# Performance work log

Measured on AMD Instinct MI355X. Metric: run time of the kernel, lower is better.

## Reference

```python
import jax, jax.numpy as jnp
import numpy as np

D_MODEL = 768
N_HEADS = 12
D_HEAD = 64
WINDOW = 16
LOOK_BACK = 1
IGNORE = -1.0e6


def look_around(x, backward=LOOK_BACK, forward=0, pad_value=0):
    # x: (b, n_windows, w, ...) -> (b, n_windows, w*(backward+forward+1), ...)
    n = x.shape[1]
    pad = [(0, 0)] * x.ndim
    pad[1] = (backward, forward)
    px = jnp.pad(x, pad, constant_values=pad_value)
    return jnp.concatenate([px[:, i:i + n] for i in range(backward + forward + 1)], axis=2)


def setup_inputs() -> dict:
    key = jax.random.key(0)
    k1, k2, k3 = jax.random.split(key, 3)
    B, T = 2, 2048
    x = jax.random.normal(k1, (B, T, D_MODEL), dtype=jnp.float32)
    W_abcde = jax.random.normal(k2, (D_MODEL, 5 * N_HEADS * D_HEAD), dtype=jnp.float32) * (1.0 / np.sqrt(D_MODEL))
    b_abcde = jnp.zeros((5 * N_HEADS * D_HEAD,), dtype=jnp.float32)
    W_O = jax.random.normal(k3, (N_HEADS * D_HEAD, D_MODEL), dtype=jnp.float32) * (1.0 / np.sqrt(N_HEADS * D_HEAD))
    b_O = jnp.zeros((D_MODEL,), dtype=jnp.float32)
    return {"x": x, "W_abcde": W_abcde, "b_abcde": b_abcde, "W_O": W_O, "b_O": b_O}


def reference(x, W_abcde, b_abcde, W_O, b_O):
    B, T, _ = x.shape
    w = WINDOW
    nw = T // w
    Ww = w * (LOOK_BACK + 1)  # look-around window length

    abcde = x @ W_abcde + b_abcde                                    # (B,T,5*H*D)
    abcde = abcde.reshape(B, T, 5, N_HEADS, D_HEAD).transpose(2, 0, 3, 1, 4)  # (5,B,H,T,D)
    a, b, c, d, e = [t.reshape(B * N_HEADS, nw, w, D_HEAD) for t in abcde]
    a_l, b_l, d_l, e_l = (look_around(t) for t in (a, b, d, e))       # (BH,nw,Ww,D)

    # causal mask, same construction as get_causal_mask (pad_value=0)
    seq = jnp.arange(T).reshape(1, nw, w)
    bb = look_around(seq)                                            # (1,nw,Ww)
    # mask[n,m,l] = (seq_n < bb_l) | (bb_l <= bb_m)
    mask = (seq[..., :, None, None] < bb[..., None, None, :]) | (bb[..., None, None, :] <= bb[..., None, :, None])

    # third-order attention scores: (BH, nw, w, Ww, Ww)
    scores = jnp.einsum('bnwd,bnmd,bnld->bnwml', c, a_l, b_l)
    scores = jnp.where(mask, IGNORE, scores)
    scores = jnp.where(scores == 0, IGNORE, scores)
    probs = jax.nn.softmax((scores / D_HEAD).reshape(B * N_HEADS, nw, w, Ww * Ww), axis=-1)
    probs = probs.reshape(scores.shape)

    z = jnp.einsum('bnwml,bnmd->bnwd', probs, d_l) + jnp.einsum('bnwml,bnld->bnwd', probs, e_l)
    z = z.reshape(B, N_HEADS, nw, w, D_HEAD).transpose(0, 2, 3, 1, 4).reshape(B, T, N_HEADS * D_HEAD)
    return z @ W_O + b_O
```

## Files before the change

kernel.cpp:

```cpp
#include <hip/hip_runtime.h>

#define T_SEQ   2048
#define NHEADS  12
#define DHEAD   64
#define WIN     16
#define WW      32
#define NWIN    128
#define DMODEL  768
#define NABCDE  3840
#define IGNORE_V (-1.0e6f)
#define PAD_K   72
#define L2E64   0.022542110013890053f
#define IGN_SC  (-22542.110013890053f)

typedef float f32x4 __attribute__((ext_vector_type(4)));
typedef _Float16 f16x8 __attribute__((ext_vector_type(8)));

__device__ __forceinline__ short f2h(float f) {
    union { _Float16 h; short s; } u;
    u.h = (_Float16)f;
    return u.s;
}

__device__ __forceinline__ void gload_lds16(const short* g, short* l) {
    __builtin_amdgcn_global_load_lds(
        (const __attribute__((address_space(1))) void*)g,
        (__attribute__((address_space(3))) void*)l,
        16, 0, 0);
}

__global__ __launch_bounds__(256) void prep_kernel(
    const float* __restrict__ x, const float* __restrict__ W_abcde,
    const float* __restrict__ W_O,
    short* __restrict__ xh, short* __restrict__ Wt, short* __restrict__ WOt)
{
    __shared__ float tile[32][33];
    const int blk = blockIdx.x;
    const int tid = threadIdx.x;

    if (blk < 1536) {
        int i = (blk * 256 + tid) * 8;
        float4 a = *reinterpret_cast<const float4*>(&x[i]);
        float4 b = *reinterpret_cast<const float4*>(&x[i + 4]);
        union { short s[8]; uint4 u; } r;
        r.s[0] = f2h(a.x); r.s[1] = f2h(a.y); r.s[2] = f2h(a.z); r.s[3] = f2h(a.w);
        r.s[4] = f2h(b.x); r.s[5] = f2h(b.y); r.s[6] = f2h(b.z); r.s[7] = f2h(b.w);
        *reinterpret_cast<uint4*>(&xh[i]) = r.u;
        return;
    }
    const float* W; short* Wo; int N, bx, by;
    if (blk < 4416) {
        int t = blk - 1536;
        W = W_abcde; Wo = Wt; N = NABCDE;
        bx = (t % 120) * 32; by = (t / 120) * 32;
    } else {
        int t = blk - 4416;
        W = W_O; Wo = WOt; N = DMODEL;
        bx = (t % 24) * 32; by = (t / 24) * 32;
    }
    const int tx = tid & 31, ty = tid >> 5;
#pragma unroll
    for (int r = 0; r < 32; r += 8)
        tile[ty + r][tx] = W[(size_t)(by + ty + r) * N + bx + tx];
    __syncthreads();
#pragma unroll
    for (int r = 0; r < 32; r += 8)
        Wo[(size_t)(bx + ty + r) * DMODEL + by + tx] = f2h(tile[tx][ty + r]);
}

__global__ __launch_bounds__(256) void gemm1_kernel(
    const short* __restrict__ A, const short* __restrict__ Bt,
    const float* __restrict__ bias, short* __restrict__ C,
    int M, int N, int K)
{
    __shared__ short As[2][128 * 32];
    __shared__ short Bs[2][128 * 32];

    const int tid  = threadIdx.x;
    const int wave = tid >> 6;
    const int lane = tid & 63;

    int bid = blockIdx.x;
    int xcd = bid & 7, t = bid >> 3;
    int sidx = t / 40, inner = t % 40;
    int sid = sidx * 8 + xcd;
    int sy = sid / 3, sx = sid % 3;
    const int ty = sy * 4 + (inner & 3);
    const int tx = sx * 10 + (inner >> 2);
    const int bm = ty * 128;
    const int bn = tx * 128;

    const int st_row = lane >> 2;
    const int st_col = (lane & 3) * 8;
    const int fr_m = lane & 15;
    const int fr_k = (lane >> 4) * 8;
    const int ko   = lane >> 4;
    const int wr = wave >> 1;
    const int wm = wr * 64;
    const int wn = (wave & 1) * 64;

    const short* gsrc[8];
    short* ldst[8];
#pragma unroll
    for (int j = 0; j < 8; ++j) {
        int c = wave * 8 + j;
        if (c < 16) {
            int kt = c >> 3, rg = c & 7;
            gsrc[j] = A + (size_t)(bm + rg * 16 + st_row) * K + kt * 32 + st_col;
            ldst[j] = &As[kt][(rg * 16) * 32];
        } else {
            int cb = c - 16;
            int kt = cb >> 3, rg = cb & 7;
            gsrc[j] = Bt + (size_t)(bn + rg * 16 + st_row) * K + kt * 32 + st_col;
            ldst[j] = &Bs[kt][(rg * 16) * 32];
        }
    }

    f32x4 acc[4][4];
#pragma unroll
    for (int mi = 0; mi < 4; ++mi)
#pragma unroll
        for (int ni = 0; ni < 4; ++ni) acc[mi][ni] = (f32x4){0.f, 0.f, 0.f, 0.f};

    for (int k0 = 0; k0 < K; k0 += 64) {
#pragma unroll
        for (int j = 0; j < 8; ++j) gload_lds16(gsrc[j] + k0, ldst[j]);
        __syncthreads();

#pragma unroll
        for (int kt = 0; kt < 2; ++kt) {
            f16x8 af[4], bfv[4];
#pragma unroll
            for (int mi = 0; mi < 4; ++mi)
                af[mi] = *reinterpret_cast<const f16x8*>(
                    &As[kt][(wm + mi * 16 + fr_m) * 32 + fr_k]);
#pragma unroll
            for (int ni = 0; ni < 4; ++ni)
                bfv[ni] = *reinterpret_cast<const f16x8*>(
                    &Bs[kt][(wn + ni * 16 + fr_m) * 32 + fr_k]);
#pragma unroll
            for (int mi = 0; mi < 4; ++mi)
#pragma unroll
                for (int ni = 0; ni < 4; ++ni)
                    acc[mi][ni] = __builtin_amdgcn_mfma_f32_16x16x32_f16(
                        af[mi], bfv[ni], acc[mi][ni], 0, 0, 0);
        }
        __syncthreads();
    }

    float bv[4];
#pragma unroll
    for (int ni = 0; ni < 4; ++ni)
        bv[ni] = bias[bn + wn + ni * 16 + fr_m];

    short* cb = &As[0][0];
#pragma unroll
    for (int half = 0; half < 2; ++half) {
        if (wr == half) {
#pragma unroll
            for (int mi = 0; mi < 4; ++mi) {
#pragma unroll
                for (int r = 0; r < 4; ++r) {
                    int row = mi * 16 + ko * 4 + r;
#pragma unroll
                    for (int ni = 0; ni < 4; ++ni)
                        cb[row * 128 + wn + ni * 16 + fr_m] =
                            f2h(acc[mi][ni][r] + bv[ni]);
                }
            }
        }
        __syncthreads();
#pragma unroll
        for (int q = 0; q < 4; ++q) {
            int f = tid + q * 256;
            int row = f >> 4, c16 = (f & 15) * 8;
            *reinterpret_cast<uint4*>(
                &C[(size_t)(bm + half * 64 + row) * N + bn + c16]) =
                *reinterpret_cast<const uint4*>(&cb[row * 128 + c16]);
        }
        __syncthreads();
    }
}

__global__ __launch_bounds__(256) void gemm_h16_64(
    const short* __restrict__ A, const short* __restrict__ Bt,
    const float* __restrict__ bias, float* __restrict__ C,
    int M, int N, int K)
{
    __shared__ short As[2][64 * 32];
    __shared__ short Bs[2][64 * 32];

    const int tid  = threadIdx.x;
    const int wave = tid >> 6;
    const int lane = tid & 63;
    const int bm = blockIdx.y * 64;
    const int bn = blockIdx.x * 64;

    const int st_row = lane >> 2;
    const int st_col = (lane & 3) * 8;
    const int fr_m = lane & 15;
    const int fr_k = (lane >> 4) * 8;
    const int wm = wave * 16;

    const short* gsrc[4];
    short* ldst[4];
#pragma unroll
    for (int j = 0; j < 4; ++j) {
        int c = wave * 4 + j;
        if (c < 8) {
            int kt = c >> 2, rg = c & 3;
            gsrc[j] = A + (size_t)(bm + rg * 16 + st_row) * K + kt * 32 + st_col;
            ldst[j] = &As[kt][(rg * 16) * 32];
        } else {
            int cb = c - 8;
            int kt = cb >> 2, rg = cb & 3;
            gsrc[j] = Bt + (size_t)(bn + rg * 16 + st_row) * K + kt * 32 + st_col;
            ldst[j] = &Bs[kt][(rg * 16) * 32];
        }
    }

    f32x4 acc[4];
#pragma unroll
    for (int ni = 0; ni < 4; ++ni) acc[ni] = (f32x4){0.f, 0.f, 0.f, 0.f};

    for (int k0 = 0; k0 < K; k0 += 64) {
#pragma unroll
        for (int j = 0; j < 4; ++j) gload_lds16(gsrc[j] + k0, ldst[j]);
        __syncthreads();

#pragma unroll
        for (int kt = 0; kt < 2; ++kt) {
            f16x8 af = *reinterpret_cast<const f16x8*>(
                &As[kt][(wm + fr_m) * 32 + fr_k]);
#pragma unroll
            for (int ni = 0; ni < 4; ++ni) {
                f16x8 bf = *reinterpret_cast<const f16x8*>(
                    &Bs[kt][(ni * 16 + fr_m) * 32 + fr_k]);
                acc[ni] = __builtin_amdgcn_mfma_f32_16x16x32_f16(
                    af, bf, acc[ni], 0, 0, 0);
            }
        }
        __syncthreads();
    }

    float bv[4];
#pragma unroll
    for (int ni = 0; ni < 4; ++ni)
        bv[ni] = bias[bn + ni * 16 + (lane & 15)];
    int rbase = bm + wm + (lane >> 4) * 4;
#pragma unroll
    for (int r = 0; r < 4; ++r) {
        size_t off = (size_t)(rbase + r) * N + bn + (lane & 15);
#pragma unroll
        for (int ni = 0; ni < 4; ++ni)
            C[off + ni * 16] = acc[ni][r] + bv[ni];
    }
}

__global__ __launch_bounds__(256) void attn_kernel(
    const short* __restrict__ abcde, short* __restrict__ z)
{
    const int blk = blockIdx.x;
    const int n  = blk & (NWIN - 1);
    const int bh = blk >> 7;
    const int b  = bh / NHEADS;
    const int h  = bh % NHEADS;

    __shared__ short sc[WIN * PAD_K];
    __shared__ short sa[WW * PAD_K];
    __shared__ short sb[WW * PAD_K];
    __shared__ short sd[WW * PAD_K];
    __shared__ short se[WW * PAD_K];
    __shared__ short epA[WIN * PAD_K];
    __shared__ float sinv[WIN];

    const int tid = threadIdx.x;
    const size_t rowbase = ((size_t)b * T_SEQ) * NABCDE;
    const int hd = h * DHEAD;

    if (tid < 128) {
        int row = tid >> 3, ch = (tid & 7) * 8;
        *reinterpret_cast<uint4*>(&sc[row * PAD_K + ch]) =
            *reinterpret_cast<const uint4*>(
                &abcde[rowbase + (size_t)(n * WIN + row) * NABCDE + 2 * DMODEL + hd + ch]);
    }
    {
        int row = tid >> 3, ch = (tid & 7) * 8;
        int t = n * WIN - WIN + row;
        uint4 va = {0u, 0u, 0u, 0u}, vb = va, vd = va, ve = va;
        if (t >= 0) {
            size_t base = rowbase + (size_t)t * NABCDE + hd + ch;
            va = *reinterpret_cast<const uint4*>(&abcde[base + 0 * DMODEL]);
            vb = *reinterpret_cast<const uint4*>(&abcde[base + 1 * DMODEL]);
            vd = *reinterpret_cast<const uint4*>(&abcde[base + 3 * DMODEL]);
            ve = *reinterpret_cast<const uint4*>(&abcde[base + 4 * DMODEL]);
        }
        *reinterpret_cast<uint4*>(&sa[row * PAD_K + ch]) = va;
        *reinterpret_cast<uint4*>(&sb[row * PAD_K + ch]) = vb;
        *reinterpret_cast<uint4*>(&sd[row * PAD_K + ch]) = vd;
        *reinterpret_cast<uint4*>(&se[row * PAD_K + ch]) = ve;
    }
    __syncthreads();

    const int wv = tid >> 6;
    const int lane = tid & 63;
    const int lc = lane & 15;
    const int ko = lane >> 4;

    f16x8 cfrag[2];
    f16x8 bfrag[2][2];
#pragma unroll
    for (int kt = 0; kt < 2; ++kt) {
        cfrag[kt] = *reinterpret_cast<const f16x8*>(
            &sc[(wv * 4 + (lc & 3)) * PAD_K + kt * 32 + ko * 8]) * (_Float16)L2E64;
        bfrag[0][kt] = *reinterpret_cast<const f16x8*>(&sb[lc * PAD_K + kt * 32 + ko * 8]);
        bfrag[1][kt] = *reinterpret_cast<const f16x8*>(&sb[(16 + lc) * PAD_K + kt * 32 + ko * 8]);
    }

    f32x4 acc[8][2];
#pragma unroll
    for (int mt = 0; mt < 8; ++mt) {
        acc[mt][0] = (f32x4){0.f, 0.f, 0.f, 0.f};
        acc[mt][1] = (f32x4){0.f, 0.f, 0.f, 0.f};
    }
    __builtin_amdgcn_s_setprio(1);
#pragma unroll
    for (int mt = 0; mt < 8; ++mt) {
#pragma unroll
        for (int kt = 0; kt < 2; ++kt) {
            f16x8 ar = *reinterpret_cast<const f16x8*>(
                &sa[(mt * 4 + (lc >> 2)) * PAD_K + kt * 32 + ko * 8]);
            f16x8 pa = cfrag[kt] * ar;
            acc[mt][0] = __builtin_amdgcn_mfma_f32_16x16x32_f16(pa, bfrag[0][kt], acc[mt][0], 0, 0, 0);
            acc[mt][1] = __builtin_amdgcn_mfma_f32_16x16x32_f16(pa, bfrag[1][kt], acc[mt][1], 0, 0, 0);
        }
    }
    __builtin_amdgcn_s_setprio(0);

    const int nbase = n * WIN;
    if (n != 0) {
#pragma unroll
        for (int lt = 0; lt < 2; ++lt) {
            const int l = lt * 16 + lc;
#pragma unroll
            for (int mt = 0; mt < 8; ++mt) {
                const bool mgt = l > (mt * 4 + ko);
#pragma unroll
                for (int reg = 0; reg < 4; ++reg) {
                    const bool keep = mgt && (wv * 4 + reg + WIN >= l);
                    float p = __builtin_amdgcn_exp2f(acc[mt][lt][reg]);
                    acc[mt][lt][reg] = keep ? p : 0.0f;
                }
            }
        }
    } else {
        int bbl_h[2]; bool keepL[2][4];
#pragma unroll
        for (int lt = 0; lt < 2; ++lt) {
            int l = lt * 16 + lc;
            bbl_h[lt] = (l < WIN) ? 0 : (l - WIN);
#pragma unroll
            for (int reg = 0; reg < 4; ++reg)
                keepL[lt][reg] = (wv * 4 + reg) >= bbl_h[lt];
        }
#pragma unroll
        for (int mt = 0; mt < 8; ++mt) {
            int m = mt * 4 + ko;
            int bbm = (m < WIN) ? 0 : (m - WIN);
#pragma unroll
            for (int lt = 0; lt < 2; ++lt) {
                bool mgt = bbl_h[lt] > bbm;
#pragma unroll
                for (int reg = 0; reg < 4; ++reg) {
                    float s = acc[mt][lt][reg];
                    if (!(keepL[lt][reg] && mgt) || s == 0.0f)
                        acc[mt][lt][reg] = IGN_SC;
                }
            }
        }
        float mx[4] = {-3.4e38f, -3.4e38f, -3.4e38f, -3.4e38f};
#pragma unroll
        for (int mt = 0; mt < 8; ++mt)
#pragma unroll
            for (int lt = 0; lt < 2; ++lt)
#pragma unroll
                for (int reg = 0; reg < 4; ++reg)
                    mx[reg] = fmaxf(mx[reg], acc[mt][lt][reg]);
#pragma unroll
        for (int reg = 0; reg < 4; ++reg) {
#pragma unroll
            for (int off = 1; off < 64; off <<= 1)
                mx[reg] = fmaxf(mx[reg], __shfl_xor(mx[reg], off, 64));
        }
#pragma unroll
        for (int mt = 0; mt < 8; ++mt)
#pragma unroll
            for (int lt = 0; lt < 2; ++lt)
#pragma unroll
                for (int reg = 0; reg < 4; ++reg)
                    acc[mt][lt][reg] = __builtin_amdgcn_exp2f(
                        acc[mt][lt][reg] - mx[reg]);
    }

    float plv[2][4];
#pragma unroll
    for (int lt = 0; lt < 2; ++lt) {
#pragma unroll
        for (int reg = 0; reg < 4; ++reg) {
            float p = acc[0][lt][reg];
#pragma unroll
            for (int mt = 1; mt < 8; ++mt) p += acc[mt][lt][reg];
            p += __shfl_xor(p, 16, 64);
            p += __shfl_xor(p, 32, 64);
            plv[lt][reg] = p;
        }
        float w  = (ko & 1) ? plv[lt][1] : plv[lt][0];
        float w2 = (ko & 1) ? plv[lt][3] : plv[lt][2];
        float ww = (ko & 2) ? w2 : w;
        epA[(wv * 4 + ko) * PAD_K + 32 + lt * 16 + lc] = f2h(ww);
    }

    {
        float s[4];
#pragma unroll
        for (int reg = 0; reg < 4; ++reg) {
            float t = plv[0][reg] + plv[1][reg];
            t += __shfl_xor(t, 1, 64);
            t += __shfl_xor(t, 2, 64);
            t += __shfl_xor(t, 4, 64);
            t += __shfl_xor(t, 8, 64);
            s[reg] = t;
        }
        if (lane == 0) {
#pragma unroll
            for (int reg = 0; reg < 4; ++reg) sinv[wv * 4 + reg] = 1.0f / s[reg];
        }
    }

    {
        float v8[8][4];
#pragma unroll
        for (int mt = 0; mt < 8; ++mt)
#pragma unroll
            for (int reg = 0; reg < 4; ++reg)
                v8[mt][reg] = acc[mt][0][reg] + acc[mt][1][reg];

        const bool s0 = lane & 1, s1 = lane & 2, s2 = lane & 4, s3 = lane & 8;
        float r1[4][4];
#pragma unroll
        for (int m2 = 0; m2 < 4; ++m2)
#pragma unroll
            for (int reg = 0; reg < 4; ++reg) {
                float u = v8[2 * m2][reg], w = v8[2 * m2 + 1][reg];
                float a = s0 ? w : u;
                float s = s0 ? u : w;
                r1[m2][reg] = a + __shfl_xor(s, 1, 64);
            }
        float r2[2][4];
#pragma unroll
        for (int m4 = 0; m4 < 2; ++m4)
#pragma unroll
            for (int reg = 0; reg < 4; ++reg) {
                float u = r1[2 * m4][reg], w = r1[2 * m4 + 1][reg];
                float a = s1 ? w : u;
                float s = s1 ? u : w;
                r2[m4][reg] = a + __shfl_xor(s, 2, 64);
            }
        float r3[4];
#pragma unroll
        for (int reg = 0; reg < 4; ++reg) {
            float u = r2[0][reg], w = r2[1][reg];
            float a = s2 ? w : u;
            float s = s2 ? u : w;
            r3[reg] = a + __shfl_xor(s, 4, 64);
        }
        float a0 = s3 ? r3[1] : r3[0];
        float q0 = s3 ? r3[0] : r3[1];
        float g0 = a0 + __shfl_xor(q0, 8, 64);
        float a1 = s3 ? r3[3] : r3[2];
        float q1 = s3 ? r3[2] : r3[3];
        float g1 = a1 + __shfl_xor(q1, 8, 64);

        int mcol = (lc & 7) * 4 + ko;
        int ib = wv * 4 + (lc >> 3);
        epA[ib * PAD_K + mcol]       = f2h(g0);
        epA[(ib + 2) * PAD_K + mcol] = f2h(g1);
    }

    const int dd = wv * 16 + lc;
    f16x8 bd, be;
    {
        unsigned dv[8], ev[8];
#pragma unroll
        for (int j = 0; j < 8; ++j) {
            dv[j] = *reinterpret_cast<const unsigned short*>(&sd[(ko * 8 + j) * PAD_K + dd]);
            ev[j] = *reinterpret_cast<const unsigned short*>(&se[(ko * 8 + j) * PAD_K + dd]);
        }
        union { unsigned u[4]; f16x8 v; } td, te;
#pragma unroll
        for (int j = 0; j < 4; ++j) {
            td.u[j] = __builtin_amdgcn_perm(dv[2 * j + 1], dv[2 * j], 0x05040100);
            te.u[j] = __builtin_amdgcn_perm(ev[2 * j + 1], ev[2 * j], 0x05040100);
        }
        bd = td.v; be = te.v;
    }
    __syncthreads();

    f16x8 apm = *reinterpret_cast<const f16x8*>(&epA[lc * PAD_K + ko * 8]);
    f16x8 apl = *reinterpret_cast<const f16x8*>(&epA[lc * PAD_K + 32 + ko * 8]);
    f32x4 zacc = (f32x4){0.f, 0.f, 0.f, 0.f};
    __builtin_amdgcn_s_setprio(1);
    zacc = __builtin_amdgcn_mfma_f32_16x16x32_f16(apm, bd, zacc, 0, 0, 0);
    zacc = __builtin_amdgcn_mfma_f32_16x16x32_f16(apl, be, zacc, 0, 0, 0);
    __builtin_amdgcn_s_setprio(0);

    short* zs = sd;
#pragma unroll
    for (int reg = 0; reg < 4; ++reg) {
        int i = ko * 4 + reg;
        zs[i * 64 + dd] = f2h(zacc[reg] * sinv[i]);
    }
    __syncthreads();
    {
        int row = tid >> 4;
        int ch  = (tid & 15) * 4;
        *reinterpret_cast<uint2*>(
            &z[((size_t)b * T_SEQ + nbase + row) * (NHEADS * DHEAD) + hd + ch]) =
            *reinterpret_cast<const uint2*>(&zs[row * 64 + ch]);
    }
}

extern "C" void kernel_launch(void* const* d_in, const int* in_sizes, int n_in,
                              void* d_out, int out_size, void* d_ws, size_t ws_size,
                              hipStream_t stream) {
    const float* x        = (const float*)d_in[0];
    const float* W_abcde  = (const float*)d_in[1];
    const float* b_abcde  = (const float*)d_in[2];
    const float* W_O      = (const float*)d_in[3];
    const float* b_O      = (const float*)d_in[4];
    float* out = (float*)d_out;

    char* ws = (char*)d_ws;
    short* abcde = (short*)ws;
    short* xh    = (short*)(ws + (size_t)31457280);
    short* Wt    = (short*)(ws + (size_t)31457280 + 6291456);
    short* WOt   = (short*)(ws + (size_t)31457280 + 6291456 + 5898240);
    short* zb    = xh;

    const int M = 2 * T_SEQ;

    prep_kernel<<<dim3(4992), dim3(256), 0, stream>>>(
        x, W_abcde, W_O, xh, Wt, WOt);

    gemm1_kernel<<<dim3(960), dim3(256), 0, stream>>>(
        xh, Wt, b_abcde, abcde, M, NABCDE, DMODEL);

    attn_kernel<<<dim3(2 * NHEADS * NWIN), dim3(256), 0, stream>>>(abcde, zb);

    gemm_h16_64<<<dim3(DMODEL / 64, M / 64), dim3(256), 0, stream>>>(
        zb, WOt, b_O, out, M, DMODEL, DMODEL);
}
```

Before: 156.3 us.

## Rewrite QKV GEMM with 256x256 tiles, 4-stage LDS pipeline and swizzle

The first projection GEMM moves from 128x128 tiles with 256 threads to 256x256 tiles with 512 threads. It adds a 4-deep LDS ring buffer with explicit vmcnt waits and raw barriers so global-to-LDS loads run ahead of the MFMA work, an XOR swizzle on LDS columns to reduce bank conflicts, and s_setprio around the MFMA block. The aim is more data reuse per tile and better hiding of load latency. The trade-off is only 240 blocks, which may underfill the CUs, plus 128 KB of LDS and high register pressure from 32 accumulators per thread.

```diff
diff --git a/kernel.cpp b/kernel.cpp
--- a/kernel.cpp
+++ b/kernel.cpp
@@ -68,117 +68,131 @@
         Wo[(size_t)(bx + ty + r) * DMODEL + by + tx] = f2h(tile[tx][ty + r]);
 }
 
-__global__ __launch_bounds__(256) void gemm1_kernel(
+__global__ __launch_bounds__(512, 2) void gemm1_kernel(
     const short* __restrict__ A, const short* __restrict__ Bt,
     const float* __restrict__ bias, short* __restrict__ C,
     int M, int N, int K)
 {
-    __shared__ short As[2][128 * 32];
-    __shared__ short Bs[2][128 * 32];
+    __shared__ short LT[4][2][8192];
 
     const int tid  = threadIdx.x;
     const int wave = tid >> 6;
     const int lane = tid & 63;
 
     int bid = blockIdx.x;
-    int xcd = bid & 7, t = bid >> 3;
-    int sidx = t / 40, inner = t % 40;
-    int sid = sidx * 8 + xcd;
-    int sy = sid / 3, sx = sid % 3;
-    const int ty = sy * 4 + (inner & 3);
-    const int tx = sx * 10 + (inner >> 2);
-    const int bm = ty * 128;
-    const int bn = tx * 128;
-
-    const int st_row = lane >> 2;
-    const int st_col = (lane & 3) * 8;
-    const int fr_m = lane & 15;
-    const int fr_k = (lane >> 4) * 8;
-    const int ko   = lane >> 4;
-    const int wr = wave >> 1;
-    const int wm = wr * 64;
-    const int wn = (wave & 1) * 64;
-
-    const short* gsrc[8];
-    short* ldst[8];
-#pragma unroll
-    for (int j = 0; j < 8; ++j) {
-        int c = wave * 8 + j;
-        if (c < 16) {
-            int kt = c >> 3, rg = c & 7;
-            gsrc[j] = A + (size_t)(bm + rg * 16 + st_row) * K + kt * 32 + st_col;
-            ldst[j] = &As[kt][(rg * 16) * 32];
-        } else {
-            int cb = c - 16;
-            int kt = cb >> 3, rg = cb & 7;
-            gsrc[j] = Bt + (size_t)(bn + rg * 16 + st_row) * K + kt * 32 + st_col;
-            ldst[j] = &Bs[kt][(rg * 16) * 32];
-        }
-    }
-
-    f32x4 acc[4][4];
-#pragma unroll
-    for (int mi = 0; mi < 4; ++mi)
+    int t = (bid & 7) * 30 + (bid >> 3);
+    const int bm = (t / 15) * 256;
+    const int bn = (t % 15) * 256;
+
+    const int wr = wave >> 2;
+    const int wc = wave & 3;
+    const int fm = lane & 15;
+    const int ko = lane >> 4;
+    const int kswz = ko ^ ((lane >> 2) & 3);
+    const int w32 = wave * 32;
+
+    const int srow = lane >> 2;
+    const int scc  = ((lane & 3) ^ ((lane >> 4) & 3)) * 8;
+    const short* gA[2]; const short* gB[2];
+#pragma unroll
+    for (int j = 0; j < 2; ++j) {
+        gA[j] = A  + (size_t)(bm + w32 + j * 16 + srow) * K + scc;
+        gB[j] = Bt + (size_t)(bn + w32 + j * 16 + srow) * K + scc;
+    }
+
+    f32x4 acc[8][4];
+#pragma unroll
+    for (int mi = 0; mi < 8; ++mi)
 #pragma unroll
         for (int ni = 0; ni < 4; ++ni) acc[mi][ni] = (f32x4){0.f, 0.f, 0.f, 0.f};
 
-    for (int k0 = 0; k0 < K; k0 += 64) {
-#pragma unroll
-        for (int j = 0; j < 8; ++j) gload_lds16(gsrc[j] + k0, ldst[j]);
+#pragma unroll
+    for (int kt = 0; kt < 3; ++kt) {
+#pragma unroll
+        for (int j = 0; j < 2; ++j) {
+            gload_lds16(gA[j] + kt * 32, &LT[kt][0][(w32 + j * 16) * 32]);
+            gload_lds16(gB[j] + kt * 32, &LT[kt][1][(w32 + j * 16) * 32]);
+        }
+    }
+
+    const int NKT = K >> 5;
+    const int nkm = NKT - 3;
+
+#define G1_STEP(KB, VMC, DOSTAGE, KS)                                          \
+    {                                                                          \
+        asm volatile("s_waitcnt vmcnt(" #VMC ")" ::: "memory");                \
+        __builtin_amdgcn_s_barrier();                                          \
+        asm volatile("" ::: "memory");                                         \
+        if (DOSTAGE) {                                                         \
+            int sb_ = (KS) & 3;                                                \
+            _Pragma("unroll")                                                  \
+            for (int j = 0; j < 2; ++j) {                                      \
+                gload_lds16(gA[j] + (KS) * 32, &LT[sb_][0][(w32 + j * 16) * 32]); \
+                gload_lds16(gB[j] + (KS) * 32, &LT[sb_][1][(w32 + j * 16) * 32]); \
+            }                                                                  \
+        }                                                                      \
+        const short* Ab_ = &LT[(KB)][0][0];                                    \
+        const short* Bb_ = &LT[(KB)][1][0];                                    \
+        f16x8 af_[8], bf_[4];                                                  \
+        _Pragma("unroll")                                                      \
+        for (int mi = 0; mi < 8; ++mi)                                         \
+            af_[mi] = *reinterpret_cast<const f16x8*>(                         \
+                &Ab_[(wr * 128 + mi * 16 + fm) * 32 + kswz * 8]);              \
+        _Pragma("unroll")                                                      \
+        for (int ni = 0; ni < 4; ++ni)                                         \
+            bf_[ni] = *reinterpret_cast<const f16x8*>(                         \
+                &Bb_[(wc * 64 + ni * 16 + fm) * 32 + kswz * 8]);               \
+        __builtin_amdgcn_s_setprio(1);                                         \
+        _Pragma("unroll")                                                      \
+        for (int mi = 0; mi < 8; ++mi)                                         \
+            _Pragma("unroll")                                                  \
+            for (int ni = 0; ni < 4; ++ni)                                     \
+                acc[mi][ni] = __builtin_amdgcn_mfma_f32_16x16x32_f16(          \
+                    af_[mi], bf_[ni], acc[mi][ni], 0, 0, 0);                   \
+        __builtin_amdgcn_s_setprio(0);                                         \
+        asm volatile("" ::: "memory");                                         \
+        __builtin_amdgcn_s_barrier();                                          \
+    }
+
+    for (int k = 0; k < nkm; ++k) {
+        G1_STEP(k & 3, 8, true, k + 3);
+    }
+    G1_STEP(nkm & 3, 8, false, 0);
+    G1_STEP((nkm + 1) & 3, 4, false, 0);
+    G1_STEP((nkm + 2) & 3, 0, false, 0);
+#undef G1_STEP
+
+    float bv[4];
+#pragma unroll
+    for (int ni = 0; ni < 4; ++ni)
+        bv[ni] = bias[bn + wc * 64 + ni * 16 + fm];
+
+    short* cb = &LT[0][0][0];
+#pragma unroll
+    for (int half = 0; half < 2; ++half) {
         __syncthreads();
-
-#pragma unroll
-        for (int kt = 0; kt < 2; ++kt) {
-            f16x8 af[4], bfv[4];
-#pragma unroll
-            for (int mi = 0; mi < 4; ++mi)
-                af[mi] = *reinterpret_cast<const f16x8*>(
-                    &As[kt][(wm + mi * 16 + fr_m) * 32 + fr_k]);
-#pragma unroll
-            for (int ni = 0; ni < 4; ++ni)
-                bfv[ni] = *reinterpret_cast<const f16x8*>(
-                    &Bs[kt][(wn + ni * 16 + fr_m) * 32 + fr_k]);
-#pragma unroll
-            for (int mi = 0; mi < 4; ++mi)
-#pragma unroll
-                for (int ni = 0; ni < 4; ++ni)
-                    acc[mi][ni] = __builtin_amdgcn_mfma_f32_16x16x32_f16(
-                        af[mi], bfv[ni], acc[mi][ni], 0, 0, 0);
-        }
-        __syncthreads();
-    }
-
-    float bv[4];
-#pragma unroll
-    for (int ni = 0; ni < 4; ++ni)
-        bv[ni] = bias[bn + wn + ni * 16 + fr_m];
-
-    short* cb = &As[0][0];
-#pragma unroll
-    for (int half = 0; half < 2; ++half) {
         if (wr == half) {
 #pragma unroll
-            for (int mi = 0; mi < 4; ++mi) {
+            for (int mi = 0; mi < 8; ++mi) {
 #pragma unroll
                 for (int r = 0; r < 4; ++r) {
-                    int row = mi * 16 + ko * 4 + r;
+                    int lrow = mi * 16 + ko * 4 + r;
 #pragma unroll
                     for (int ni = 0; ni < 4; ++ni)
-                        cb[row * 128 + wn + ni * 16 + fr_m] =
+                        cb[lrow * 256 + wc * 64 + ni * 16 + fm] =
                             f2h(acc[mi][ni][r] + bv[ni]);
                 }
             }
         }
         __syncthreads();
 #pragma unroll
-        for (int q = 0; q < 4; ++q) {
-            int f = tid + q * 256;
-            int row = f >> 4, c16 = (f & 15) * 8;
+        for (int q = 0; q < 8; ++q) {
+            int f = tid + q * 512;
+            int row = f >> 5, c16 = (f & 31) * 8;
             *reinterpret_cast<uint4*>(
-                &C[(size_t)(bm + half * 64 + row) * N + bn + c16]) =
-                *reinterpret_cast<const uint4*>(&cb[row * 128 + c16]);
-        }
-        __syncthreads();
+                &C[(size_t)(bm + half * 128 + row) * N + bn + c16]) =
+                *reinterpret_cast<const uint4*>(&cb[row * 256 + c16]);
+        }
     }
 }
 
@@ -552,7 +566,7 @@
     prep_kernel<<<dim3(4992), dim3(256), 0, stream>>>(
         x, W_abcde, W_O, xh, Wt, WOt);
 
-    gemm1_kernel<<<dim3(960), dim3(256), 0, stream>>>(
+    gemm1_kernel<<<dim3(240), dim3(512), 0, stream>>>(
         xh, Wt, b_abcde, abcde, M, NABCDE, DMODEL);
 
     attn_kernel<<<dim3(2 * NHEADS * NWIN), dim3(256), 0, stream>>>(abcde, zb);
```

After: 147.9 us. 5.4% less time.
